# Performance work log

Measured on AMD Instinct MI355X. Metric: run time of the kernel, lower is better.

The kernel has to match this reference:

```python
import jax, jax.numpy as jnp
import numpy as np

N_NODES = 20000
N_EDGES = 320000
N_GRAPHS = 256
D = 256
L = 4
EPS = 1e-5


def setup_inputs() -> dict:
    key = jax.random.key(0)
    ks = jax.random.split(key, 20)
    x = jax.random.normal(ks[0], (N_NODES, D), dtype=jnp.float32)
    edge_index = jax.random.randint(ks[1], (2, N_EDGES), 0, N_NODES, dtype=jnp.int64)
    batch = jnp.sort(jax.random.randint(ks[2], (N_NODES,), 0, N_GRAPHS, dtype=jnp.int64))
    s = 1.0 / np.sqrt(D)
    Wl = jax.random.uniform(ks[3], (L, D, D), jnp.float32, -s, s)
    bl = jax.random.uniform(ks[4], (L, D), jnp.float32, -s, s)
    Wr = jax.random.uniform(ks[5], (L, D, D), jnp.float32, -s, s)
    gamma = jnp.ones((L, D), jnp.float32)
    beta = jnp.zeros((L, D), jnp.float32)
    fc1_w = jax.random.uniform(ks[6], (D, 128), jnp.float32, -s, s)
    fc1_b = jax.random.uniform(ks[7], (128,), jnp.float32, -s, s)
    s2 = 1.0 / np.sqrt(128)
    fc2_w = jax.random.uniform(ks[8], (128, 64), jnp.float32, -s2, s2)
    fc2_b = jax.random.uniform(ks[9], (64,), jnp.float32, -s2, s2)
    s3 = 1.0 / np.sqrt(64)
    fc3_w = jax.random.uniform(ks[10], (64, 10), jnp.float32, -s3, s3)
    fc3_b = jax.random.uniform(ks[11], (10,), jnp.float32, -s3, s3)
    return dict(x=x, edge_index=edge_index, batch=batch, Wl=Wl, bl=bl, Wr=Wr,
                gamma=gamma, beta=beta, fc1_w=fc1_w, fc1_b=fc1_b,
                fc2_w=fc2_w, fc2_b=fc2_b, fc3_w=fc3_w, fc3_b=fc3_b)


def reference(x, edge_index, batch, Wl, bl, Wr, gamma, beta,
              fc1_w, fc1_b, fc2_w, fc2_b, fc3_w, fc3_b):
    src, dst = edge_index[0], edge_index[1]
    # in-degree for mean aggregation (zero-degree nodes -> 0 aggregate)
    deg = jax.ops.segment_sum(jnp.ones((src.shape[0],), x.dtype), dst, num_segments=N_NODES)
    inv_deg = jnp.where(deg > 0, 1.0 / jnp.maximum(deg, 1.0), 0.0)[:, None]
    for i in range(L):
        # SAGEConv: mean-aggregate neighbors, then lin_l(agg) + lin_r(x)
        agg = jax.ops.segment_sum(x[src], dst, num_segments=N_NODES) * inv_deg
        h = agg @ Wl[i] + bl[i] + x @ Wr[i]
        # BatchNorm (training mode: biased batch statistics over nodes)
        mu = jnp.mean(h, axis=0)
        var = jnp.mean(jnp.square(h - mu), axis=0)
        h = (h - mu) * jax.lax.rsqrt(var + EPS) * gamma[i] + beta[i]
        x = jax.nn.relu(h)
    # global_mean_pool over graphs
    cnt = jax.ops.segment_sum(jnp.ones((N_NODES,), x.dtype), batch, num_segments=N_GRAPHS)
    g = jax.ops.segment_sum(x, batch, num_segments=N_GRAPHS) / jnp.maximum(cnt, 1.0)[:, None]
    # MLP classifier: 256 -> 128 -> 64 -> 10
    g = jax.nn.relu(g @ fc1_w + fc1_b)
    g = jax.nn.relu(g @ fc2_w + fc2_b)
    return g @ fc3_w + fc3_b
```

## Files before the change

kernel.cpp:

```cpp
#include <hip/hip_runtime.h>
#include <hip/hip_bf16.h>

#define NN 20000
#define NE 320000
#define NG 256
#define DD 256
#define NL 4
#define NBX2 157

typedef __attribute__((ext_vector_type(8))) short short8;
typedef __attribute__((ext_vector_type(4))) float float4_t;

__device__ __forceinline__ int ld_idx(const int* __restrict__ p, int i, int f64) {
    return f64 ? p[2 * i] : p[i];
}

__device__ __forceinline__ float bf2f(ushort u) {
    return __uint_as_float(((unsigned)u) << 16);
}

__device__ __forceinline__ ushort f2bf(float f) {
    __hip_bfloat16 b = __float2bfloat16(f);
    return *(ushort*)&b;
}


__global__ void k_init(const int* __restrict__ ei, const int* __restrict__ batch,
                       const ushort* __restrict__ x, int* __restrict__ flags,
                       int* __restrict__ deg) {
    int gid = blockIdx.x * 256 + threadIdx.x;
    for (int i = gid; i < NN; i += gridDim.x * 256) deg[i] = 0;
    if (blockIdx.x == 0) {
        __shared__ int cnt0, cnt1, weird;
        int t = threadIdx.x;
        if (t == 0) { cnt0 = 0; cnt1 = 0; weird = 0; }
        __syncthreads();
        for (int tt = t; tt < 512; tt += 256) {
            if (ei[2 * tt + 1] != 0) atomicAdd(&cnt0, 1);
            int i = tt * 9;
            if (batch[2 * i + 1] != 0) atomicAdd(&cnt1, 1);
#pragma unroll
            for (int j = 0; j < 16; j++) {
                ushort v = x[tt * 16 + j];
                if (((v >> 7) & 0xFF) >= 0xC0) atomicAdd(&weird, 1);
            }
        }
        __syncthreads();
        if (t == 0) {
            flags[0] = (cnt0 == 0) ? 1 : 0;
            flags[1] = (cnt1 == 0) ? 1 : 0;
            flags[2] = (weird == 0) ? 1 : 0;
        }
    }
}


#define POFF_BL   0
#define POFF_GA   1024
#define POFF_BE   2048
#define POFF_F1W  3072
#define POFF_F1B  35840
#define POFF_F2W  35968
#define POFF_F2B  44160
#define POFF_F3W  44224
#define POFF_F3B  44864
#define PTOT      44874

#define NB_CVT8   2500
#define NB_FRAG   2048
#define NB_CVTP   176
#define NB_DEG    1250
#define NB_GST    79
#define B_FRAG    (NB_CVT8)
#define B_CVTP    (B_FRAG + NB_FRAG)
#define B_DEG     (B_CVTP + NB_CVTP)
#define B_GST     (B_DEG + NB_DEG)
#define NB_PREP   (B_GST + NB_GST)


__global__ __launch_bounds__(256) void k_prep(
    const void* __restrict__ x_in, const void* __restrict__ WL,
    const void* __restrict__ WR, const int* __restrict__ ei,
    const int* __restrict__ batch,
    const void* s0, const void* s1, const void* s2, const void* s3,
    const void* s4, const void* s5, const void* s6, const void* s7, const void* s8,
    ushort* __restrict__ xcan, ushort* __restrict__ wtL, ushort* __restrict__ wtR,
    ushort* __restrict__ pcan, int* __restrict__ deg, int* __restrict__ gstart,
    const int* __restrict__ fl) {
    int blk = blockIdx.x;
    int t = threadIdx.x;
    if (blk < B_FRAG) {
        int i = blk * 256 + t;
        if (fl[2]) {
            *(int4*)(xcan + (size_t)i * 8) = ((const int4*)x_in)[i];
        } else {
            const float* f = (const float*)x_in + (size_t)i * 8;
            ushort ov[8];
#pragma unroll
            for (int d = 0; d < 8; d++) ov[d] = f2bf(f[d]);
            *(int4*)(xcan + (size_t)i * 8) = *(int4*)ov;
        }
    } else if (blk < B_CVTP) {
        int idx = (blk - B_FRAG) * 256 + t;
        int half = idx >> 18;
        int id = idx & 0x3FFFF;
        int within = id & 0xFFFF;
        int lmat = id >> 16;
        int fblk = within >> 9;
        int lane = (within >> 3) & 63;
        int e = within & 7;
        int n = (fblk >> 3) * 16 + (lane & 15);
        int k = (fblk & 7) * 32 + (lane >> 4) * 8 + e;
        const void* W = half ? WR : WL;
        ushort* Wt = half ? wtR : wtL;
        size_t src = ((size_t)lmat << 16) + (k << 8) + n;
        Wt[id] = fl[2] ? ((const ushort*)W)[src] : f2bf(((const float*)W)[src]);
    } else if (blk < B_DEG) {
        int i = (blk - B_CVTP) * 256 + t;
        if (i >= PTOT) return;
        const int offs[10] = {POFF_BL, POFF_GA, POFF_BE, POFF_F1W, POFF_F1B,
                              POFF_F2W, POFF_F2B, POFF_F3W, POFF_F3B, PTOT};
        const void* srcs[9] = {s0, s1, s2, s3, s4, s5, s6, s7, s8};
        int seg = 0;
#pragma unroll
        for (int k = 1; k < 9; k++) if (i >= offs[k]) seg = k;
        int local = i - offs[seg];
        if (fl[2]) pcan[i] = ((const ushort*)srcs[seg])[local];
        else       pcan[i] = f2bf(((const float*)srcs[seg])[local]);
    } else if (blk < B_GST) {
        int e = (blk - B_DEG) * 256 + t;
        if (e < NE) {
            int src = ld_idx(ei, e, fl[0]);
            int dst = ld_idx(ei, NE + e, fl[0]);
            if ((unsigned)dst < NN && (unsigned)src < NN) atomicAdd(&deg[dst], 1);
        }
    } else {
        int i = (blk - B_GST) * 256 + t;
        if (i >= NN) return;
        int b = ld_idx(batch, i, fl[1]);
        int bp = (i == 0) ? -1 : ld_idx(batch, i - 1, fl[1]);
        for (int g = bp + 1; g <= b; g++)
            if ((unsigned)g <= NG) gstart[g] = i;
        if (i == NN - 1)
            for (int g = b + 1; g <= NG; g++) gstart[g] = NN;
    }
}


__global__ void k_scan3(const int* __restrict__ deg, int* __restrict__ rowst,
                        int* __restrict__ cursor, float* __restrict__ invdeg) {
    __shared__ int part[1024];
    int t = threadIdx.x;
    const int per = (NN + 1023) / 1024;
    int lo = t * per;
    int hi = lo + per; if (hi > NN) hi = NN;
    int s = 0;
    for (int i = lo; i < hi; i++) s += deg[i];
    part[t] = s;
    __syncthreads();
    for (int off = 1; off < 1024; off <<= 1) {
        int v = (t >= off) ? part[t - off] : 0;
        __syncthreads();
        part[t] += v;
        __syncthreads();
    }
    if (t == 1023) rowst[NN] = part[1023];
    int run = part[t] - s;
    for (int i = lo; i < hi; i++) {
        int d = deg[i];
        rowst[i] = run;
        cursor[i] = run;
        invdeg[i] = d > 0 ? 1.0f / (float)d : 0.0f;
        run += d;
    }
}

__global__ void k_fill(const int* __restrict__ ei, int* __restrict__ cursor,
                       int* __restrict__ csr, const int* __restrict__ fl) {
    int e = blockIdx.x * 256 + threadIdx.x;
    if (e < NE) {
        int src = ld_idx(ei, e, fl[0]);
        int dst = ld_idx(ei, NE + e, fl[0]);
        if ((unsigned)dst < NN && (unsigned)src < NN) {
            int p = atomicAdd(&cursor[dst], 1);
            if ((unsigned)p < NE) csr[p] = src;
        }
    }
}


template <int BNF>
__global__ __launch_bounds__(256) void k_agg4(
    const ushort* __restrict__ X, const int* __restrict__ rs,
    const int* __restrict__ csr, const float* __restrict__ invdeg,
    const float* __restrict__ bnsc, const float* __restrict__ bnsh,
    ushort* __restrict__ AGG) {
    int node = blockIdx.x * 4 + (threadIdx.x >> 6);
    if (node >= NN) return;
    int h = (threadIdx.x >> 5) & 1;
    int j = threadIdx.x & 31;
    float sc[8], sh[8];
    if (BNF) {
        float4 a0 = *(const float4*)(bnsc + j * 8);
        float4 a1 = *(const float4*)(bnsc + j * 8 + 4);
        float4 b0 = *(const float4*)(bnsh + j * 8);
        float4 b1 = *(const float4*)(bnsh + j * 8 + 4);
        sc[0] = a0.x; sc[1] = a0.y; sc[2] = a0.z; sc[3] = a0.w;
        sc[4] = a1.x; sc[5] = a1.y; sc[6] = a1.z; sc[7] = a1.w;
        sh[0] = b0.x; sh[1] = b0.y; sh[2] = b0.z; sh[3] = b0.w;
        sh[4] = b1.x; sh[5] = b1.y; sh[6] = b1.z; sh[7] = b1.w;
    }
    int e0 = rs[node], e1 = rs[node + 1];
    float acc[8] = {};
    int e = e0 + h;
    for (; e + 14 < e1; e += 16) {
        int4 v[8];
#pragma unroll
        for (int r = 0; r < 8; r++) {
            int s = csr[e + 2 * r];
            v[r] = *(const int4*)(X + (size_t)s * DD + j * 8);
        }
#pragma unroll
        for (int r = 0; r < 8; r++) {
            const ushort* u = (const ushort*)&v[r];
#pragma unroll
            for (int d = 0; d < 8; d++) {
                float x = bf2f(u[d]);
                if (BNF) x = fmaxf(x * sc[d] + sh[d], 0.0f);
                acc[d] += x;
            }
        }
    }
    for (; e + 2 < e1; e += 4) {
        int sA = csr[e], sB = csr[e + 2];
        int4 vA = *(const int4*)(X + (size_t)sA * DD + j * 8);
        int4 vB = *(const int4*)(X + (size_t)sB * DD + j * 8);
        const ushort* uA = (const ushort*)&vA;
        const ushort* uB = (const ushort*)&vB;
#pragma unroll
        for (int d = 0; d < 8; d++) {
            float xA = bf2f(uA[d]), xB = bf2f(uB[d]);
            if (BNF) {
                xA = fmaxf(xA * sc[d] + sh[d], 0.0f);
                xB = fmaxf(xB * sc[d] + sh[d], 0.0f);
            }
            acc[d] += xA + xB;
        }
    }
    for (; e < e1; e += 2) {
        int s = csr[e];
        int4 v = *(const int4*)(X + (size_t)s * DD + j * 8);
        const ushort* u = (const ushort*)&v;
#pragma unroll
        for (int d = 0; d < 8; d++) {
            float x = bf2f(u[d]);
            if (BNF) x = fmaxf(x * sc[d] + sh[d], 0.0f);
            acc[d] += x;
        }
    }
#pragma unroll
    for (int d = 0; d < 8; d++)
        acc[d] += __shfl_down(acc[d], 32);
    if (h == 0) {
        float inv = invdeg[node];
        ushort ov[8];
#pragma unroll
        for (int d = 0; d < 8; d++) ov[d] = f2bf(acc[d] * inv);
        *(int4*)(AGG + (size_t)node * DD + j * 8) = *(int4*)ov;
    }
}


template <int BNF>
__global__ __launch_bounds__(256) void k_gemm5(
    const ushort* __restrict__ A1, const ushort* __restrict__ A2,
    const ushort* __restrict__ WtF1, const ushort* __restrict__ WtF2,
    const ushort* __restrict__ bias,
    const float* __restrict__ bnsc, const float* __restrict__ bnsh,
    ushort* __restrict__ H, float* __restrict__ psum, float* __restrict__ psq) {
    __shared__ ushort Als[128][40];
    __shared__ float colsum[128];
    __shared__ float colsq[128];
    const int m0 = blockIdx.x * 128;
    const int n0 = blockIdx.y * 128;
    const int tid = threadIdx.x;
    const int w = tid >> 6, l = tid & 63, lr = l & 15, q = l >> 4;
    const int wm = (w >> 1) * 64, wn = (w & 1) * 64;
    float4_t acc[4][4] = {};

    const int srow = tid >> 1;
    const int sce = (tid & 1) * 16;
    const int nb8 = ((n0 + wn) >> 4) * 8;

    for (int mat = 0; mat < 2; ++mat) {
        const ushort* A = mat ? A2 : A1;
        const ushort* Wf = mat ? WtF2 : WtF1;
        for (int k0 = 0; k0 < 256; k0 += 32) {
            int ar = m0 + srow; if (ar >= NN) ar = NN - 1;
            int4 av0 = *(const int4*)(A + (size_t)ar * DD + k0 + sce);
            int4 av1 = *(const int4*)(A + (size_t)ar * DD + k0 + sce + 8);
            if (BNF && mat == 1) {
                float scv[16], shv[16];
#pragma unroll
                for (int g = 0; g < 4; g++) {
                    float4 s4 = *(const float4*)(bnsc + k0 + sce + g * 4);
                    float4 h4 = *(const float4*)(bnsh + k0 + sce + g * 4);
                    scv[g*4] = s4.x; scv[g*4+1] = s4.y; scv[g*4+2] = s4.z; scv[g*4+3] = s4.w;
                    shv[g*4] = h4.x; shv[g*4+1] = h4.y; shv[g*4+2] = h4.z; shv[g*4+3] = h4.w;
                }
                ushort* u0 = (ushort*)&av0;
                ushort* u1 = (ushort*)&av1;
#pragma unroll
                for (int d = 0; d < 8; d++) {
                    u0[d] = f2bf(fmaxf(bf2f(u0[d]) * scv[d] + shv[d], 0.0f));
                    u1[d] = f2bf(fmaxf(bf2f(u1[d]) * scv[8 + d] + shv[8 + d], 0.0f));
                }
            }
            *(int4*)&Als[srow][sce] = av0;
            *(int4*)&Als[srow][sce + 8] = av1;
            const ushort* bbase = Wf + (((size_t)(nb8 + (k0 >> 5))) << 9) + l * 8;
            short8 bf[4];
#pragma unroll
            for (int in = 0; in < 4; in++)
                bf[in] = *(const short8*)(bbase + in * 4096);
            __syncthreads();
            short8 af[4];
#pragma unroll
            for (int im = 0; im < 4; im++)
                af[im] = *(const short8*)&Als[wm + im * 16 + lr][q * 8];
#pragma unroll
            for (int im = 0; im < 4; im++)
#pragma unroll
                for (int in = 0; in < 4; in++)
                    acc[im][in] = __builtin_amdgcn_mfma_f32_16x16x32_bf16(
                        af[im], bf[in], acc[im][in], 0, 0, 0);
            __syncthreads();
        }
    }
    if (tid < 128) { colsum[tid] = 0.0f; colsq[tid] = 0.0f; }
    __syncthreads();

    int mbase = m0 + wm + q * 4;
#pragma unroll
    for (int in = 0; in < 4; in++) {
        int n = n0 + wn + in * 16 + lr;
        float b = bf2f(bias[n]);
        float s = 0.0f, s2 = 0.0f;
#pragma unroll
        for (int im = 0; im < 4; im++) {
#pragma unroll
            for (int i = 0; i < 4; i++) {
                int m = mbase + im * 16 + i;
                if (m < NN) {
                    float hv = acc[im][in][i] + b;
                    ushort hb = f2bf(hv);
                    H[(size_t)m * DD + n] = hb;
                    float hq = bf2f(hb);
                    s += hq;
                    s2 += hq * hq;
                }
            }
        }
        s += __shfl_xor(s, 16);  s += __shfl_xor(s, 32);
        s2 += __shfl_xor(s2, 16); s2 += __shfl_xor(s2, 32);
        if (q == 0) {
            atomicAdd(&colsum[wn + in * 16 + lr], s);
            atomicAdd(&colsq[wn + in * 16 + lr], s2);
        }
    }
    __syncthreads();
    if (tid < 128) {
        psum[(size_t)blockIdx.x * DD + n0 + tid] = colsum[tid];
        psq[(size_t)blockIdx.x * DD + n0 + tid] = colsq[tid];
    }
}


__global__ __launch_bounds__(64) void k_bnfinal3(
    const float* __restrict__ psum, const float* __restrict__ psq,
    const ushort* __restrict__ gamma, const ushort* __restrict__ beta,
    float* __restrict__ scale, float* __restrict__ shift) {
    int c = blockIdx.x;
    int t = threadIdx.x;
    float s = 0.0f, s2 = 0.0f;
    for (int b = t; b < NBX2; b += 64) {
        s += psum[(size_t)b * DD + c];
        s2 += psq[(size_t)b * DD + c];
    }
#pragma unroll
    for (int o = 32; o; o >>= 1) {
        s += __shfl_down(s, o);
        s2 += __shfl_down(s2, o);
    }
    if (t == 0) {
        float mu = s * (1.0f / NN);
        float var = s2 * (1.0f / NN) - mu * mu;
        if (var < 0.0f) var = 0.0f;
        float rstd = rsqrtf(var + 1e-5f);
        float g = bf2f(gamma[c]);
        float b2 = bf2f(beta[c]);
        scale[c] = g * rstd;
        shift[c] = b2 - mu * g * rstd;
    }
}


__global__ __launch_bounds__(256) void k_head(
    const ushort* __restrict__ Hb, const float* __restrict__ scale,
    const float* __restrict__ shift, const int* __restrict__ gstart,
    const ushort* __restrict__ fc1w, const ushort* __restrict__ fc1b,
    const ushort* __restrict__ fc2w, const ushort* __restrict__ fc2b,
    const ushort* __restrict__ fc3w, const ushort* __restrict__ fc3b,
    void* __restrict__ out, const int* __restrict__ fl) {
    __shared__ float g[256];
    __shared__ float h1[128];
    __shared__ float h2[64];
    int gid = blockIdx.x;
    int t = threadIdx.x;
    int s0 = gstart[gid], e = gstart[gid + 1];
    float sc = scale[t], sh = shift[t];
    float acc = 0.0f;
    for (int i = s0; i < e; i++)
        acc += fmaxf(bf2f(Hb[(size_t)i * DD + t]) * sc + sh, 0.0f);
    g[t] = acc / fmaxf((float)(e - s0), 1.0f);
    __syncthreads();
    if (t < 128) {
        float a = bf2f(fc1b[t]);
        for (int k = 0; k < 256; k++)
            a += g[k] * bf2f(fc1w[k * 128 + t]);
        h1[t] = fmaxf(a, 0.0f);
    }
    __syncthreads();
    if (t < 64) {
        float a2 = bf2f(fc2b[t]);
        for (int k = 0; k < 128; k++)
            a2 += h1[k] * bf2f(fc2w[k * 64 + t]);
        h2[t] = fmaxf(a2, 0.0f);
    }
    __syncthreads();
    if (t < 10) {
        float a3 = bf2f(fc3b[t]);
        for (int k = 0; k < 64; k++)
            a3 += h2[k] * bf2f(fc3w[k * 10 + t]);
        if (fl[2]) ((__hip_bfloat16*)out)[gid * 10 + t] = __float2bfloat16(a3);
        else       ((float*)out)[gid * 10 + t] = a3;
    }
}


static inline char* bump(char*& p, size_t n) {
    char* r = p;
    p += (n + 255) & ~(size_t)255;
    return r;
}

extern "C" void kernel_launch(void* const* d_in, const int* in_sizes, int n_in,
                              void* d_out, int out_size, void* d_ws, size_t ws_size,
                              hipStream_t stream) {
    const void* x_in  = d_in[0];
    const int*  ei    = (const int*)d_in[1];
    const int*  batch = (const int*)d_in[2];
    const void* Wl    = d_in[3];
    const void* bl    = d_in[4];
    const void* Wr    = d_in[5];
    const void* gamma = d_in[6];
    const void* beta  = d_in[7];

    char* p = (char*)d_ws;
    int*    flags    = (int*)bump(p, 256);
    ushort* wtL      = (ushort*)bump(p, (size_t)NL * 65536 * 2);
    ushort* wtR      = (ushort*)bump(p, (size_t)NL * 65536 * 2);
    ushort* xcan     = (ushort*)bump(p, (size_t)NN * DD * 2);
    ushort* pcan     = (ushort*)bump(p, (size_t)PTOT * 2);
    int*    deg      = (int*)bump(p, NN * 4);
    int*    rowst    = (int*)bump(p, (NN + 1) * 4);
    int*    cursor   = (int*)bump(p, NN * 4);
    float*  invdeg   = (float*)bump(p, NN * 4);
    int*    csr      = (int*)bump(p, NE * 4);
    int*    gstart   = (int*)bump(p, (NG + 1) * 4);
    ushort* agg      = (ushort*)bump(p, (size_t)NN * DD * 2);
    ushort* hb0      = (ushort*)bump(p, (size_t)NN * DD * 2);
    ushort* hb1      = (ushort*)bump(p, (size_t)NN * DD * 2);
    float*  psum     = (float*)bump(p, (size_t)NBX2 * DD * 4);
    float*  psq      = (float*)bump(p, (size_t)NBX2 * DD * 4);
    float*  scale    = (float*)bump(p, DD * 4);
    float*  shift    = (float*)bump(p, DD * 4);

    if ((size_t)(p - (char*)d_ws) > ws_size) return;

    ushort* blc = pcan + POFF_BL;
    ushort* gac = pcan + POFF_GA;
    ushort* bec = pcan + POFF_BE;
    ushort* f1w = pcan + POFF_F1W;
    ushort* f1b = pcan + POFF_F1B;
    ushort* f2w = pcan + POFF_F2W;
    ushort* f2b = pcan + POFF_F2B;
    ushort* f3w = pcan + POFF_F3W;
    ushort* f3b = pcan + POFF_F3B;

    k_init<<<80, 256, 0, stream>>>(ei, batch, (const ushort*)x_in, flags, deg);
    k_prep<<<NB_PREP, 256, 0, stream>>>(
        x_in, Wl, Wr, ei, batch,
        bl, gamma, beta, d_in[8], d_in[9], d_in[10], d_in[11], d_in[12], d_in[13],
        xcan, wtL, wtR, pcan, deg, gstart, flags);
    k_scan3<<<1, 1024, 0, stream>>>(deg, rowst, cursor, invdeg);
    k_fill<<<(NE + 255) / 256, 256, 0, stream>>>(ei, cursor, csr, flags);

    ushort* hbuf[2] = {hb0, hb1};
    const ushort* xsrc = xcan;
    for (int l = 0; l < NL; l++) {
        ushort* hdst = hbuf[l & 1];
        if (l == 0) {
            k_agg4<0><<<(NN + 3) / 4, 256, 0, stream>>>(xsrc, rowst, csr, invdeg,
                                                        scale, shift, agg);
            k_gemm5<0><<<dim3(NBX2, 2), 256, 0, stream>>>(
                agg, xsrc, wtL, wtR, blc, scale, shift, hdst, psum, psq);
        } else {
            k_agg4<1><<<(NN + 3) / 4, 256, 0, stream>>>(xsrc, rowst, csr, invdeg,
                                                        scale, shift, agg);
            k_gemm5<1><<<dim3(NBX2, 2), 256, 0, stream>>>(
                agg, xsrc, wtL + (size_t)l * 65536, wtR + (size_t)l * 65536,
                blc + l * DD, scale, shift, hdst, psum, psq);
        }
        k_bnfinal3<<<DD, 64, 0, stream>>>(psum, psq, gac + l * DD, bec + l * DD,
                                          scale, shift);
        xsrc = hdst;
    }

    k_head<<<NG, 256, 0, stream>>>(xsrc, scale, shift, gstart,
                                   f1w, f1b, f2w, f2b, f3w, f3b, d_out, flags);
}
```

Measured before the change: 407.8 us.

## Parallelize CSR degree prefix scan with per-bucket partial counts

Replaces the single-block 1024-thread serial-chunk scan over node degrees with a two-stage scan. Degree counting now also accumulates per-256-node bucket totals into 8 replicated partial arrays. A tiny kernel scans those bucket totals, and a 79-block kernel does the intra-bucket scan and writes rowst, cursor and invdeg. This removes a long single-block serial pass, at the cost of extra atomics in degree counting and one more launch.

```diff
diff --git a/kernel.cpp b/kernel.cpp
--- a/kernel.cpp
+++ b/kernel.cpp
@@ -7,6 +7,7 @@
 #define DD 256
 #define NL 4
 #define NBX2 157
+#define NBKT 79
 
 typedef __attribute__((ext_vector_type(8))) short short8;
 typedef __attribute__((ext_vector_type(4))) float float4_t;
@@ -27,9 +28,10 @@
 
 __global__ void k_init(const int* __restrict__ ei, const int* __restrict__ batch,
                        const ushort* __restrict__ x, int* __restrict__ flags,
-                       int* __restrict__ deg) {
+                       int* __restrict__ deg, int* __restrict__ bpart) {
     int gid = blockIdx.x * 256 + threadIdx.x;
     for (int i = gid; i < NN; i += gridDim.x * 256) deg[i] = 0;
+    if (gid < 8 * 80) bpart[gid] = 0;
     if (blockIdx.x == 0) {
         __shared__ int cnt0, cnt1, weird;
         int t = threadIdx.x;
@@ -85,8 +87,8 @@
     const void* s0, const void* s1, const void* s2, const void* s3,
     const void* s4, const void* s5, const void* s6, const void* s7, const void* s8,
     ushort* __restrict__ xcan, ushort* __restrict__ wtL, ushort* __restrict__ wtR,
-    ushort* __restrict__ pcan, int* __restrict__ deg, int* __restrict__ gstart,
-    const int* __restrict__ fl) {
+    ushort* __restrict__ pcan, int* __restrict__ deg, int* __restrict__ bpart,
+    int* __restrict__ gstart, const int* __restrict__ fl) {
     int blk = blockIdx.x;
     int t = threadIdx.x;
     if (blk < B_FRAG) {
@@ -132,7 +134,10 @@
         if (e < NE) {
             int src = ld_idx(ei, e, fl[0]);
             int dst = ld_idx(ei, NE + e, fl[0]);
-            if ((unsigned)dst < NN && (unsigned)src < NN) atomicAdd(&deg[dst], 1);
+            if ((unsigned)dst < NN && (unsigned)src < NN) {
+                atomicAdd(&deg[dst], 1);
+                atomicAdd(&bpart[(blk & 7) * 80 + (dst >> 8)], 1);
+            }
         }
     } else {
         int i = (blk - B_GST) * 256 + t;
@@ -147,31 +152,46 @@
 }
 
 
-__global__ void k_scan3(const int* __restrict__ deg, int* __restrict__ rowst,
-                        int* __restrict__ cursor, float* __restrict__ invdeg) {
-    __shared__ int part[1024];
+__global__ __launch_bounds__(128) void k_scanB(const int* __restrict__ bpart,
+                                               int* __restrict__ bpref,
+                                               int* __restrict__ rowst) {
+    __shared__ int part[128];
     int t = threadIdx.x;
-    const int per = (NN + 1023) / 1024;
-    int lo = t * per;
-    int hi = lo + per; if (hi > NN) hi = NN;
     int s = 0;
-    for (int i = lo; i < hi; i++) s += deg[i];
+    if (t < NBKT)
+        for (int c = 0; c < 8; c++) s += bpart[c * 80 + t];
     part[t] = s;
     __syncthreads();
-    for (int off = 1; off < 1024; off <<= 1) {
+    for (int off = 1; off < 128; off <<= 1) {
         int v = (t >= off) ? part[t - off] : 0;
         __syncthreads();
         part[t] += v;
         __syncthreads();
     }
-    if (t == 1023) rowst[NN] = part[1023];
-    int run = part[t] - s;
-    for (int i = lo; i < hi; i++) {
-        int d = deg[i];
-        rowst[i] = run;
-        cursor[i] = run;
-        invdeg[i] = d > 0 ? 1.0f / (float)d : 0.0f;
-        run += d;
+    if (t < NBKT) bpref[t] = part[t] - s;
+    if (t == NBKT - 1) { bpref[NBKT] = part[t]; rowst[NN] = part[t]; }
+}
+
+__global__ __launch_bounds__(256) void k_scanC(
+    const int* __restrict__ deg, const int* __restrict__ bpref,
+    int* __restrict__ rowst, int* __restrict__ cursor, float* __restrict__ invdeg) {
+    __shared__ int part[256];
+    int b = blockIdx.x, t = threadIdx.x;
+    int node = b * 256 + t;
+    int d = (node < NN) ? deg[node] : 0;
+    part[t] = d;
+    __syncthreads();
+    for (int off = 1; off < 256; off <<= 1) {
+        int v = (t >= off) ? part[t - off] : 0;
+        __syncthreads();
+        part[t] += v;
+        __syncthreads();
+    }
+    if (node < NN) {
+        int o = bpref[b] + part[t] - d;
+        rowst[node] = o;
+        cursor[node] = o;
+        invdeg[node] = d > 0 ? 1.0f / (float)d : 0.0f;
     }
 }
 
@@ -473,6 +493,8 @@
     ushort* xcan     = (ushort*)bump(p, (size_t)NN * DD * 2);
     ushort* pcan     = (ushort*)bump(p, (size_t)PTOT * 2);
     int*    deg      = (int*)bump(p, NN * 4);
+    int*    bpart    = (int*)bump(p, 8 * 80 * 4);
+    int*    bpref    = (int*)bump(p, (NBKT + 1) * 4);
     int*    rowst    = (int*)bump(p, (NN + 1) * 4);
     int*    cursor   = (int*)bump(p, NN * 4);
     float*  invdeg   = (float*)bump(p, NN * 4);
@@ -498,12 +520,13 @@
     ushort* f3w = pcan + POFF_F3W;
     ushort* f3b = pcan + POFF_F3B;
 
-    k_init<<<80, 256, 0, stream>>>(ei, batch, (const ushort*)x_in, flags, deg);
+    k_init<<<80, 256, 0, stream>>>(ei, batch, (const ushort*)x_in, flags, deg, bpart);
     k_prep<<<NB_PREP, 256, 0, stream>>>(
         x_in, Wl, Wr, ei, batch,
         bl, gamma, beta, d_in[8], d_in[9], d_in[10], d_in[11], d_in[12], d_in[13],
-        xcan, wtL, wtR, pcan, deg, gstart, flags);
-    k_scan3<<<1, 1024, 0, stream>>>(deg, rowst, cursor, invdeg);
+        xcan, wtL, wtR, pcan, deg, bpart, gstart, flags);
+    k_scanB<<<1, 128, 0, stream>>>(bpart, bpref, rowst);
+    k_scanC<<<NBKT, 256, 0, stream>>>(deg, bpref, rowst, cursor, invdeg);
     k_fill<<<(NE + 255) / 256, 256, 0, stream>>>(ei, cursor, csr, flags);
 
     ushort* hbuf[2] = {hb0, hb1};
```

After: 413.9 us. No clear change (+1.5%).
